# Kernel tuning notes

Measured on AMD Instinct MI355X. Metric: run time of the kernel, lower is better.

The kernel has to match this reference:

```python
import jax, jax.numpy as jnp
import numpy as np
from jax import lax

S, B, T, H, FH, FU = 8, 256, 90, 256, 14, 76
IN_H, IN_F, IN_U = 16, 16, 4


def _cell(x, h, c, Wih, Whh, b):
    # x:[S,B,in] h,c:[S,B,H] Wih:[S,4H,in] Whh:[S,4H,H] b:[S,4H]
    g = jnp.einsum('sbi,sgi->sbg', x, Wih) + jnp.einsum('sbh,sgh->sbg', h, Whh) + b[:, None, :]
    i, f, gg, o = jnp.split(g, 4, axis=-1)
    c = jax.nn.sigmoid(f) * c + jax.nn.sigmoid(i) * jnp.tanh(gg)
    h = jax.nn.sigmoid(o) * jnp.tanh(c)
    return h, c


def _encode(x_seq, params):
    # x_seq:[T,S,B,in]; stacked LSTM, zero initial state (torch nn.LSTM default)
    hs, cs = [], []
    inp = x_seq
    for (Wih, Whh, b) in params:
        h0 = jnp.zeros((x_seq.shape[1], x_seq.shape[2], Whh.shape[-1]), x_seq.dtype)

        def step(carry, x, Wih=Wih, Whh=Whh, b=b):
            h, c = _cell(x, carry[0], carry[1], Wih, Whh, b)
            return (h, c), h

        (h, c), inp = lax.scan(step, (h0, h0), inp)
        hs.append(h); cs.append(c)
    return jnp.stack(hs), jnp.stack(cs)  # [L,S,B,H]


def _decode(x_seq, params, h0, c0, level, win, wout, gW, gb, adj, flow_std):
    L = len(params)

    def step(carry, x):
        hs, cs, lev = carry
        inp = x
        nh, nc = [], []
        for l in range(L):
            h, c = _cell(inp, hs[l], cs[l], *params[l])
            inp = h; nh.append(h); nc.append(c)
        # headers_in: Linear(H+1 -> H, no bias) + ReLU (dropout is eval no-op)
        feat = jnp.concatenate([inp, lev], axis=-1)            # [S,B,H+1]
        hin = jax.nn.relu(jnp.einsum('sbf,shf->sbh', feat, win))
        # GraphConvolution: adj @ (X W) + b over the site axis
        graphed = jnp.einsum('st,tbk->sbk', adj, jnp.einsum('sbh,hk->sbk', hin, gW)) + gb
        # headers_out: ReLU + Linear(H -> 1, no bias)
        flow = jnp.einsum('sbh,soh->sbo', jax.nn.relu(graphed), wout)  # [S,B,1]
        lev = lev + flow * flow_std[:, None, None]
        return (jnp.stack(nh), jnp.stack(nc), lev), flow[..., 0]
    (hs, cs, lev), flows = lax.scan(step, (h0, c0, level), x_seq)
    return hs, cs, lev, flows  # flows: [T,S,B]


def setup_inputs() -> dict:
    key = jax.random.key(0)
    ks = iter(jax.random.split(key, 40))
    sc = 1.0 / np.sqrt(H)

    def u(shape):
        return jax.random.uniform(next(ks), shape, jnp.float32, -sc, sc)

    inp = {
        'x_d': jax.random.normal(next(ks), (S, B, T, IN_H), jnp.float32),
        'x_f': jax.random.normal(next(ks), (S, B, FH, IN_F), jnp.float32),
        'x_ff': jax.random.normal(next(ks), (S, B, FU, IN_U), jnp.float32),
        'level0': jax.random.uniform(next(ks), (S, B, 1), jnp.float32),
        'flow_std': jax.random.uniform(next(ks), (S,), jnp.float32, 0.5, 2.0),
    }
    # adjacency: chain edges + self loops (diag=True, digraph=False)
    adj = np.zeros((S, S), dtype=np.float32)
    for i in range(S - 1):
        adj[i, i + 1] = 1.0
    adj += np.eye(S, dtype=np.float32)
    inp['adj'] = jnp.asarray(adj)
    for pfx, in0 in [('enc', IN_H), ('df', IN_F), ('du', IN_U)]:
        inp[pfx + '_Wih0'] = u((S, 4 * H, in0))
        inp[pfx + '_Whh0'] = u((S, 4 * H, H))
        inp[pfx + '_b0'] = u((S, 4 * H))
        inp[pfx + '_Wih1'] = u((S, 4 * H, H))
        inp[pfx + '_Whh1'] = u((S, 4 * H, H))
        inp[pfx + '_b1'] = u((S, 4 * H))
    inp['win'] = u((S, H, H + 1))
    inp['wout'] = u((S, 1, H))
    inp['gW'] = u((H, H))
    inp['gb'] = u((H,))
    return inp


def reference(x_d, x_f, x_ff, level0, flow_std, adj,
              enc_Wih0, enc_Whh0, enc_b0, enc_Wih1, enc_Whh1, enc_b1,
              df_Wih0, df_Whh0, df_b0, df_Wih1, df_Whh1, df_b1,
              du_Wih0, du_Whh0, du_b0, du_Wih1, du_Whh1, du_b1,
              win, wout, gW, gb):
    enc_p = [(enc_Wih0, enc_Whh0, enc_b0), (enc_Wih1, enc_Whh1, enc_b1)]
    df_p = [(df_Wih0, df_Whh0, df_b0), (df_Wih1, df_Whh1, df_b1)]
    du_p = [(du_Wih0, du_Whh0, du_b0), (du_Wih1, du_Whh1, du_b1)]
    # encode historic sequence per site
    h, c = _encode(jnp.transpose(x_d, (2, 0, 1, 3)), enc_p)
    # forecast-horizon decode with graph mixing each step
    h, c, lev, f1 = _decode(jnp.transpose(x_f, (2, 0, 1, 3)), df_p, h, c,
                            level0, win, wout, gW, gb, adj, flow_std)
    # future-horizon decode continues from the same state
    h, c, lev, f2 = _decode(jnp.transpose(x_ff, (2, 0, 1, 3)), du_p, h, c,
                            lev, win, wout, gW, gb, adj, flow_std)
    flows = jnp.concatenate([f1, f2], axis=0)      # [FH+FU, S, B]
    return jnp.transpose(flows, (2, 0, 1))         # [B, target_horizon, S]
```

## Files before the change

### kernel.cpp

```cpp
#include <hip/hip_runtime.h>

typedef unsigned short u16;
typedef __bf16 bf16_t;
typedef bf16_t bf16x8 __attribute__((ext_vector_type(8)));
typedef float f32x4 __attribute__((ext_vector_type(4)));
typedef unsigned int u32x4 __attribute__((ext_vector_type(4)));

#define DEV static __device__ __forceinline__
#define RLX __ATOMIC_RELAXED
#define AGT __HIP_MEMORY_SCOPE_AGENT

DEV u16 f2bf(float f){ unsigned u = __float_as_uint(f); return (u16)((u + 0x7fffu + ((u>>16)&1u))>>16); }
DEV float bf2f(u16 b){ return __uint_as_float(((unsigned)b)<<16); }
DEV float sigf(float x){ return 1.0f/(1.0f+__expf(-x)); }
DEV float tanhf_(float x){ float e = __expf(2.0f*x); return 1.0f - 2.0f/(e+1.0f); }

union FragU { bf16x8 v; u16 u[8]; u32x4 q; };

DEV void ldg16_nw(u32x4 r[16], const void* b0, const void* b1){
  asm volatile(
    "global_load_dwordx4 %0,  %16, off sc0 sc1\n\t"
    "global_load_dwordx4 %1,  %16, off offset:64 sc0 sc1\n\t"
    "global_load_dwordx4 %2,  %16, off offset:128 sc0 sc1\n\t"
    "global_load_dwordx4 %3,  %16, off offset:192 sc0 sc1\n\t"
    "global_load_dwordx4 %4,  %16, off offset:256 sc0 sc1\n\t"
    "global_load_dwordx4 %5,  %16, off offset:320 sc0 sc1\n\t"
    "global_load_dwordx4 %6,  %16, off offset:384 sc0 sc1\n\t"
    "global_load_dwordx4 %7,  %16, off offset:448 sc0 sc1\n\t"
    "global_load_dwordx4 %8,  %17, off sc0 sc1\n\t"
    "global_load_dwordx4 %9,  %17, off offset:64 sc0 sc1\n\t"
    "global_load_dwordx4 %10, %17, off offset:128 sc0 sc1\n\t"
    "global_load_dwordx4 %11, %17, off offset:192 sc0 sc1\n\t"
    "global_load_dwordx4 %12, %17, off offset:256 sc0 sc1\n\t"
    "global_load_dwordx4 %13, %17, off offset:320 sc0 sc1\n\t"
    "global_load_dwordx4 %14, %17, off offset:384 sc0 sc1\n\t"
    "global_load_dwordx4 %15, %17, off offset:448 sc0 sc1"
    : "=&v"(r[0]), "=&v"(r[1]), "=&v"(r[2]), "=&v"(r[3]),
      "=&v"(r[4]), "=&v"(r[5]), "=&v"(r[6]), "=&v"(r[7]),
      "=&v"(r[8]), "=&v"(r[9]), "=&v"(r[10]), "=&v"(r[11]),
      "=&v"(r[12]), "=&v"(r[13]), "=&v"(r[14]), "=&v"(r[15])
    : "v"(b0), "v"(b1)
    : "memory");
}
DEV void wait_vm16(){ asm volatile("s_waitcnt vmcnt(16)" ::: "memory"); __builtin_amdgcn_sched_barrier(0); }
DEV void wait_vm0(){ asm volatile("s_waitcnt vmcnt(0)" ::: "memory"); __builtin_amdgcn_sched_barrier(0); }

DEV void ldg8f_sc(u32x4 r[8], float& lv, const void* b0, const float* lp){
  asm volatile(
    "global_load_dwordx4 %0, %9, off sc0 sc1\n\t"
    "global_load_dwordx4 %1, %9, off offset:64 sc0 sc1\n\t"
    "global_load_dwordx4 %2, %9, off offset:128 sc0 sc1\n\t"
    "global_load_dwordx4 %3, %9, off offset:192 sc0 sc1\n\t"
    "global_load_dwordx4 %4, %9, off offset:256 sc0 sc1\n\t"
    "global_load_dwordx4 %5, %9, off offset:320 sc0 sc1\n\t"
    "global_load_dwordx4 %6, %9, off offset:384 sc0 sc1\n\t"
    "global_load_dwordx4 %7, %9, off offset:448 sc0 sc1\n\t"
    "global_load_dword %8, %10, off sc0 sc1\n\t"
    "s_waitcnt vmcnt(0)"
    : "=&v"(r[0]), "=&v"(r[1]), "=&v"(r[2]), "=&v"(r[3]),
      "=&v"(r[4]), "=&v"(r[5]), "=&v"(r[6]), "=&v"(r[7]), "=&v"(lv)
    : "v"(b0), "v"(lp) : "memory");
}
DEV float ldf_sc(const float* p){
  float r;
  asm volatile("global_load_dword %0, %1, off sc0 sc1\n\ts_waitcnt vmcnt(0)"
               : "=&v"(r) : "v"(p) : "memory");
  return r;
}
DEV void stg16_sc(void* p, u32x4 v){
  asm volatile("global_store_dwordx4 %0, %1, off sc0 sc1" :: "v"(p), "v"(v) : "memory");
}
DEV void stf_sc(float* p, float v){
  asm volatile("global_store_dword %0, %1, off sc0 sc1" :: "v"(p), "v"(v) : "memory");
}
DEV unsigned ld_spin_ic(const unsigned* p){
  unsigned r;
  asm volatile("global_load_dword %0, %1, off sc0 sc1\n\ts_waitcnt vmcnt(0)"
               : "=&v"(r) : "v"(p) : "memory");
  return r;
}

struct PArgs {
  const u16 *whh0[3], *wih0p[3], *whh1[3], *wih1[3];
  const float *b0[3], *b1[3];
  const float *x[3];
  const u16 *winH; const float *winLev;
  const u16 *gT;
  const float *gb, *wout, *adj, *fstd;
  u16 *h0a, *h0b, *h1a, *h1b;
  u16 *hgA, *hgB;
  float *levA, *levB;
  float *out;
  unsigned *bar;
  int T[3]; int IN[3];
};

DEV void pinW256(const u16* Wsite, int gt, u16* lds, int tid){
#pragma unroll
  for (int it = 0; it < 8; ++it){
    int flat = it*512 + tid;
    int n = flat >> 5, ks = flat & 31;
    int j = (n >> 5)*256 + gt*32 + (n & 31);
    bf16x8 v = *reinterpret_cast<const bf16x8*>(Wsite + (size_t)j*256 + ks*8);
    int sl = ks ^ (n & 7);
    *reinterpret_cast<bf16x8*>(lds + n*256 + sl*8) = v;
  }
}
DEV void pinWp(const u16* wpSite, int gt, u16* lds, int tid){
  int n = tid >> 2, ks = tid & 3;
  int j = (n >> 5)*256 + gt*32 + (n & 31);
  bf16x8 v = *reinterpret_cast<const bf16x8*>(wpSite + (size_t)j*32 + ks*8);
  int sl = ks ^ (n & 3);
  *reinterpret_cast<bf16x8*>(lds + n*32 + sl*8) = v;
}
DEV void pinWin(const u16* winH, int s, int gt, u16* lds, int tid){
#pragma unroll
  for (int it = 0; it < 2; ++it){
    int flat = it*512 + tid;
    int nn = flat >> 5, ks = flat & 31;
    bf16x8 v = *reinterpret_cast<const bf16x8*>(winH + ((size_t)s*256 + gt*32 + nn)*256 + ks*8);
    int sl = ks ^ (nn & 7);
    *reinterpret_cast<bf16x8*>(lds + nn*256 + sl*8) = v;
  }
}

DEV void seg_mfma(const u16* ldsW, const u32x4 a[16], f32x4 acc[2][4],
                  int l15, int l4, int nh){
#pragma unroll
  for (int ck = 0; ck < 8; ++ck){
#pragma unroll
    for (int mf = 0; mf < 2; ++mf){
      FragU af; af.q = a[mf*8 + ck];
#pragma unroll
      for (int q = 0; q < 4; ++q){
        int n = q*32 + nh*16 + l15;
        int sl = (ck*4 + l4) ^ (n & 7);
        acc[mf][q] = __builtin_amdgcn_mfma_f32_16x16x32_bf16(
            af.v, *reinterpret_cast<const bf16x8*>(ldsW + n*256 + sl*8), acc[mf][q], 0,0,0);
      }
    }
  }
}

DEV void cell_epi2(const float bb[4], float* cR, u16* hOutSite,
                   int rowBase, int hcb, int lane, u16* wscr, const f32x4 acc[2][4]){
  int l15 = lane & 15, l4 = lane >> 4;
#pragma unroll
  for (int mf = 0; mf < 2; ++mf)
#pragma unroll
    for (int r = 0; r < 4; ++r){
      float gi = acc[mf][0][r] + bb[0];
      float gf = acc[mf][1][r] + bb[1];
      float gg = acc[mf][2][r] + bb[2];
      float go = acc[mf][3][r] + bb[3];
      float cn = sigf(gf)*cR[mf*4+r] + sigf(gi)*tanhf_(gg);
      cR[mf*4+r] = cn;
      wscr[(mf*16 + l4*4 + r)*16 + l15] = f2bf(sigf(go)*tanhf_(cn));
    }
  asm volatile("s_waitcnt lgkmcnt(0)" ::: "memory");
  u32x4 v = *reinterpret_cast<const u32x4*>(wscr + lane*8);
  stg16_sc(hOutSite + (size_t)(rowBase + (lane>>1))*256 + hcb + (lane&1)*8, v);
}

__global__ __launch_bounds__(512, 2) void k_persist(PArgs A){
  extern __shared__ char smem[];
  u16* lds0 = (u16*)smem;
  u16* lds1 = (u16*)(smem + 65536);
  u16* ldsWin = (u16*)(smem + 65536 + 8192);
  u16* scratch = (u16*)(smem + 131072);
  float (*red)[16] = (float(*)[16])(smem + 139264);
  __shared__ unsigned pollE[8], pollD[8];

  const int bid = blockIdx.x, tid = threadIdx.x;
  const int w = tid >> 6, lane = tid & 63, l15 = lane & 15, l4 = lane >> 4;
  const int s = bid & 7, fam = (bid >> 3) & 1, sub = bid >> 4;
  const int bt = sub & 1, gt = sub >> 1;
  const int mt = w & 3, nh = w >> 2;
  const int rowBase = bt*128 + mt*32;
  const int hcb = gt*32 + nh*16;
  const size_t sOff = (size_t)s*65536;
  u16* wscr = scratch + w*512;

  auto offA = [](int ss, int bb){ return (unsigned)((ss*2 + bb)*64); };
  auto offB = [](int ss, int bb){ return (unsigned)(1024 + (ss*2 + bb)*64); };
  if (tid == 0){
    pollE[0] = offA(s, bt); pollE[1] = offB(s, bt);
#pragma unroll
    for (int i = 2; i < 8; ++i) pollE[i] = pollE[0];
    if (fam == 0){
      pollD[0] = offA(s, bt);
      pollD[1] = offB(s, 0); pollD[2] = offB(s, 1);
      pollD[3] = (s > 0) ? offB(s-1, 0) : pollD[0];
      pollD[4] = (s > 0) ? offB(s-1, 1) : pollD[0];
      pollD[5] = pollD[0]; pollD[6] = pollD[0]; pollD[7] = pollD[0];
    } else {
      pollD[0] = offA(s, 0); pollD[1] = offA(s, 1);
      pollD[2] = offB(s, 0); pollD[3] = offB(s, 1);
      if (s < 7){
        pollD[4] = offA(s+1, 0); pollD[5] = offA(s+1, 1);
        pollD[6] = offB(s+1, 0); pollD[7] = offB(s+1, 1);
      } else {
        pollD[4] = pollD[0]; pollD[5] = pollD[0];
        pollD[6] = pollD[0]; pollD[7] = pollD[0];
      }
    }
  }
  unsigned* myCnt = A.bar + ((fam == 0) ? offA(s, bt) : offB(s, bt));
  __syncthreads();

  float cR[8];
#pragma unroll
  for (int i = 0; i < 8; ++i) cR[i] = 0.f;

  unsigned gen = 0;
  const int gb0[3] = {0, 90, 104};

  for (int ph = 0; ph < 3; ++ph){
    const int T = A.T[ph];
    const int IN = A.IN[ph];
    const bool dec = (ph > 0);
    const int SS = T + (dec ? 3 : 1);
    const int tdb = (ph == 2) ? 14 : 0;

    float bb[4];
    if (fam == 0){
      pinW256(A.whh0[ph] + (size_t)s*262144, gt, lds0, tid);
      pinWp  (A.wih0p[ph] + (size_t)s*32768, gt, lds1, tid);
      pinWin (A.winH, s, gt, ldsWin, tid);
      const float* bS = A.b0[ph] + s*1024;
#pragma unroll
      for (int g = 0; g < 4; ++g) bb[g] = bS[g*256 + hcb + l15];
    } else {
      pinW256(A.whh1[ph] + (size_t)s*262144, gt, lds0, tid);
      pinW256(A.wih1[ph] + (size_t)s*262144, gt, lds1, tid);
      const float* bS = A.b1[ph] + s*1024;
#pragma unroll
      for (int g = 0; g < 4; ++g) bb[g] = bS[g*256 + hcb + l15];
    }
    __syncthreads();

    for (int ss = 0; ss < SS; ++ss){
      if (w == 0){
        unsigned off = (dec ? pollD : pollE)[lane & 7];
        const unsigned* p = A.bar + off;
        unsigned tgt = 8u * gen;
        for (;;){
          unsigned v = ld_spin_ic(p);
          if (__all((int)(v >= tgt))) break;
          __builtin_amdgcn_s_sleep(1);
        }
      }
      __syncthreads();

      if (fam == 0){
        if (ss < T){
          int t = ss, g0 = gb0[ph] + t;
          const u16* h0in = ((g0 & 1) ? A.h0b : A.h0a) + sOff;
          u16* h0out = ((g0 & 1) ? A.h0a : A.h0b) + sOff;
          f32x4 acc[2][4];
#pragma unroll
          for (int mf = 0; mf < 2; ++mf)
#pragma unroll
            for (int q = 0; q < 4; ++q) acc[mf][q] = (f32x4){0.f,0.f,0.f,0.f};
          u32x4 a[16];
          ldg16_nw(a, h0in + (size_t)(rowBase + l15)*256 + l4*8,
                      h0in + (size_t)(rowBase + 16 + l15)*256 + l4*8);
          FragU xa[2];
#pragma unroll
          for (int mf = 0; mf < 2; ++mf){
#pragma unroll
            for (int e = 0; e < 8; ++e) xa[mf].u[e] = 0;
            const float* xrow = A.x[ph] + ((size_t)(s*256 + rowBase + mf*16 + l15)*T + t)*IN;
            if (IN == 16){
              if (l4 < 2){
                float4 u0 = reinterpret_cast<const float4*>(xrow)[l4*2];
                float4 u1 = reinterpret_cast<const float4*>(xrow)[l4*2+1];
                xa[mf].u[0]=f2bf(u0.x); xa[mf].u[1]=f2bf(u0.y); xa[mf].u[2]=f2bf(u0.z); xa[mf].u[3]=f2bf(u0.w);
                xa[mf].u[4]=f2bf(u1.x); xa[mf].u[5]=f2bf(u1.y); xa[mf].u[6]=f2bf(u1.z); xa[mf].u[7]=f2bf(u1.w);
              }
            } else {
              if (l4 == 0){
                float4 u0 = *reinterpret_cast<const float4*>(xrow);
                xa[mf].u[0]=f2bf(u0.x); xa[mf].u[1]=f2bf(u0.y); xa[mf].u[2]=f2bf(u0.z); xa[mf].u[3]=f2bf(u0.w);
              }
            }
          }
          wait_vm0();
          seg_mfma(lds0, a, acc, l15, l4, nh);
#pragma unroll
          for (int mf = 0; mf < 2; ++mf)
#pragma unroll
            for (int q = 0; q < 4; ++q){
              int n = q*32 + nh*16 + l15;
              int sl = l4 ^ (n & 3);
              acc[mf][q] = __builtin_amdgcn_mfma_f32_16x16x32_bf16(
                  xa[mf].v, *reinterpret_cast<const bf16x8*>(lds1 + n*32 + sl*8), acc[mf][q], 0,0,0);
            }
          cell_epi2(bb, cR, h0out, rowBase, hcb, lane, wscr, acc);
        }
        if (dec){
          int th = ss - 2;
          if (th >= 0 && th < T){
            int g = gb0[ph] + th, tdec = tdb + th;
            const u16* h1cur = ((g & 1) ? A.h1a : A.h1b) + sOff;
            u16* hg = ((tdec & 1) ? A.hgB : A.hgA) + sOff;
            f32x4 a2[2];
            a2[0] = (f32x4){0.f,0.f,0.f,0.f}; a2[1] = a2[0];
            u32x4 a[16];
            ldg16_nw(a, h1cur + (size_t)(rowBase + l15)*256 + l4*8,
                        h1cur + (size_t)(rowBase + 16 + l15)*256 + l4*8);
            wait_vm0();
#pragma unroll
            for (int ck = 0; ck < 8; ++ck)
#pragma unroll
              for (int mf = 0; mf < 2; ++mf){
                FragU af; af.q = a[mf*8 + ck];
                int n = nh*16 + l15;
                int sl = (ck*4 + l4) ^ (n & 7);
                a2[mf] = __builtin_amdgcn_mfma_f32_16x16x32_bf16(
                    af.v, *reinterpret_cast<const bf16x8*>(ldsWin + n*256 + sl*8), a2[mf], 0,0,0);
              }
#pragma unroll
            for (int mf = 0; mf < 2; ++mf)
#pragma unroll
              for (int r = 0; r < 4; ++r)
                wscr[(mf*16 + l4*4 + r)*16 + l15] = f2bf(a2[mf][r]);
            asm volatile("s_waitcnt lgkmcnt(0)" ::: "memory");
            u32x4 v = *reinterpret_cast<const u32x4*>(wscr + lane*8);
            stg16_sc(hg + (size_t)(rowBase + (lane>>1))*256 + hcb + (lane&1)*8, v);
          }
        }
      } else {
        int t = ss - 1;
        if (t >= 0 && t < T){
          int g = gb0[ph] + t;
          const u16* h1in = ((g & 1) ? A.h1b : A.h1a) + sOff;
          u16* h1out = ((g & 1) ? A.h1a : A.h1b) + sOff;
          const u16* h0cur = ((g & 1) ? A.h0a : A.h0b) + sOff;
          f32x4 acc[2][4];
#pragma unroll
          for (int mf = 0; mf < 2; ++mf)
#pragma unroll
            for (int q = 0; q < 4; ++q) acc[mf][q] = (f32x4){0.f,0.f,0.f,0.f};
          u32x4 a0[16], a1[16];
          ldg16_nw(a0, h1in + (size_t)(rowBase + l15)*256 + l4*8,
                       h1in + (size_t)(rowBase + 16 + l15)*256 + l4*8);
          ldg16_nw(a1, h0cur + (size_t)(rowBase + l15)*256 + l4*8,
                       h0cur + (size_t)(rowBase + 16 + l15)*256 + l4*8);
          wait_vm16();
          seg_mfma(lds0, a0, acc, l15, l4, nh);
          wait_vm0();
          seg_mfma(lds1, a1, acc, l15, l4, nh);
          cell_epi2(bb, cR, h1out, rowBase, hcb, lane, wscr, acc);
        }
        if (dec){
          int tgl = ss - 3;
          if (tgl >= 0 && tgl < T){
            int tg = tdb + tgl;
            const u16* hgb16 = (tg & 1) ? A.hgB : A.hgA;
            const float* levc = (tg & 1) ? A.levB : A.levA;
            float* levn = (tg & 1) ? A.levA : A.levB;
            int brow0 = sub*16;
            f32x4 acc[2];
            acc[0] = (f32x4){0.f,0.f,0.f,0.f}; acc[1] = acc[0];
            for (int ts = 0; ts < 8; ++ts){
              float av = A.adj[s*8 + ts];
              if (av == 0.f) continue;
              float lv;
              u32x4 hv[8];
              ldg8f_sc(hv, lv, hgb16 + (size_t)ts*65536 + (size_t)(brow0 + l15)*256 + l4*8,
                       levc + ts*256 + brow0 + l15);
              const float* wlB = A.winLev + ts*256 + l4*8;
#pragma unroll
              for (int ck = 0; ck < 8; ++ck){
                FragU hr; hr.q = hv[ck];
                float4 w0 = *reinterpret_cast<const float4*>(wlB + ck*32);
                float4 w1 = *reinterpret_cast<const float4*>(wlB + ck*32 + 4);
                float wls[8] = {w0.x,w0.y,w0.z,w0.w,w1.x,w1.y,w1.z,w1.w};
                FragU af;
#pragma unroll
                for (int e = 0; e < 8; ++e)
                  af.u[e] = f2bf(fmaxf(bf2f(hr.u[e]) + lv*wls[e], 0.f) * av);
#pragma unroll
                for (int q = 0; q < 2; ++q){
                  int n = (w*2+q)*16 + l15;
                  bf16x8 bfr = *reinterpret_cast<const bf16x8*>(A.gT + (size_t)n*256 + ck*32 + l4*8);
                  acc[q] = __builtin_amdgcn_mfma_f32_16x16x32_bf16(af.v, bfr, acc[q], 0,0,0);
                }
              }
            }
            float part[4] = {0.f,0.f,0.f,0.f};
            const float* woS = A.wout + s*256;
#pragma unroll
            for (int q = 0; q < 2; ++q){
              int m = (w*2+q)*16 + l15;
              float gbv = A.gb[m], wo = woS[m];
#pragma unroll
              for (int r = 0; r < 4; ++r) part[r] += fmaxf(acc[q][r] + gbv, 0.f) * wo;
            }
#pragma unroll
            for (int d = 1; d < 16; d <<= 1)
#pragma unroll
              for (int r = 0; r < 4; ++r) part[r] += __shfl_xor(part[r], d, 64);
            if (l15 == 0)
#pragma unroll
              for (int r = 0; r < 4; ++r) red[w][l4*4+r] = part[r];
            __syncthreads();
            if (tid < 16){
              float flow = 0.f;
#pragma unroll
              for (int ww = 0; ww < 8; ++ww) flow += red[ww][tid];
              int b = brow0 + tid;
              A.out[(size_t)b*720 + tg*8 + s] = flow;
              float lvo = ldf_sc(levc + s*256 + b);
              stf_sc(levn + s*256 + b, lvo + flow * A.fstd[s]);
            }
          }
        }
      }
      asm volatile("s_waitcnt vmcnt(0)" ::: "memory");
      __syncthreads();
      if (tid == 0) __hip_atomic_fetch_add(myCnt, 1u, RLX, AGT);
      ++gen;
    }
  }
}

struct Cvt9Args { const float* s[9]; u16* d[9]; };
__global__ void k_cvt9(Cvt9Args A){
  size_t i = (size_t)blockIdx.x*256 + threadIdx.x;
  int t = (int)(i >> 21); size_t r = i & 2097151u;
  A.d[t][r] = f2bf(A.s[t][r]);
}
struct Pad3Args { const float* s[3]; u16* d[3]; int kx[3]; };
__global__ void k_pad3(Pad3Args A){
  size_t i = (size_t)blockIdx.x*256 + threadIdx.x;
  int t = (int)(i >> 18); int r = (int)(i & 262143u);
  int row = r >> 5, col = r & 31;
  int kx = A.kx[t];
  A.d[t][r] = (col < kx) ? f2bf(A.s[t][(size_t)row*kx + col]) : (u16)0;
}
__global__ void k_win(const float* win, u16* winH, float* winLev){
  size_t i = (size_t)blockIdx.x*256 + threadIdx.x;
  if (i >= (size_t)8*256*257) return;
  int k = (int)(i % 257); size_t sm = i / 257;
  float v = win[i];
  if (k < 256) winH[sm*256 + k] = f2bf(v);
  else winLev[sm] = v;
}
__global__ void k_gt(const float* gW, u16* gT){
  int i = blockIdx.x*256 + threadIdx.x;
  int h = i >> 8, k = i & 255;
  gT[(size_t)k*256 + h] = f2bf(gW[i]);
}

extern "C" void kernel_launch(void* const* d_in, const int* in_sizes, int n_in,
                              void* d_out, int out_size, void* d_ws, size_t ws_size,
                              hipStream_t stream){
  const float* x_d    = (const float*)d_in[0];
  const float* x_f    = (const float*)d_in[1];
  const float* x_ff   = (const float*)d_in[2];
  const float* level0 = (const float*)d_in[3];
  const float* fstd   = (const float*)d_in[4];
  const float* adj    = (const float*)d_in[5];
  const float* W[18];
  for (int i = 0; i < 18; i++) W[i] = (const float*)d_in[6+i];
  const float* win  = (const float*)d_in[24];
  const float* wout = (const float*)d_in[25];
  const float* gW   = (const float*)d_in[26];
  const float* gb   = (const float*)d_in[27];

  char* base = (char*)d_ws;
  size_t off = 0;
  auto alloc = [&](size_t bytes)->void*{
    void* r = base + off;
    off += (bytes + 255) & ~(size_t)255;
    return r;
  };
  u16* wb[9]; for (int i = 0; i < 9; i++) wb[i] = (u16*)alloc((size_t)2097152*2);
  u16* wp[3]; for (int i = 0; i < 3; i++) wp[i] = (u16*)alloc((size_t)262144*2);
  u16* winH = (u16*)alloc((size_t)524288*2);
  u16* gT   = (u16*)alloc((size_t)65536*2);
  float* winLev = (float*)alloc((size_t)2048*4);
  u16* h0a = (u16*)alloc((size_t)524288*2);
  u16* h0b = (u16*)alloc((size_t)524288*2);
  u16* h1a = (u16*)alloc((size_t)524288*2);
  u16* h1b = (u16*)alloc((size_t)524288*2);
  u16* hgA = (u16*)alloc((size_t)524288*2);
  u16* hgB = (u16*)alloc((size_t)524288*2);
  float* levA = (float*)alloc((size_t)2048*4);
  float* levB = (float*)alloc((size_t)2048*4);
  unsigned* bar = (unsigned*)alloc(16384);

  Cvt9Args c9;
  const float* c9s[9] = { W[1], W[4], W[3],  W[7], W[10], W[9],  W[13], W[16], W[15] };
  for (int i = 0; i < 9; i++){ c9.s[i] = c9s[i]; c9.d[i] = wb[i]; }
  k_cvt9<<<73728,256,0,stream>>>(c9);

  Pad3Args p3;
  const float* p3s[3] = { W[0], W[6], W[12] };
  int kx3[3] = {16,16,4};
  for (int i = 0; i < 3; i++){ p3.s[i] = p3s[i]; p3.d[i] = wp[i]; p3.kx[i] = kx3[i]; }
  k_pad3<<<3072,256,0,stream>>>(p3);

  k_win<<<2057,256,0,stream>>>(win, winH, winLev);
  k_gt<<<256,256,0,stream>>>(gW, gT);

  (void)hipMemsetAsync(h0a, 0, (size_t)524288*2, stream);
  (void)hipMemsetAsync(h1a, 0, (size_t)524288*2, stream);
  (void)hipMemsetAsync(bar, 0, 16384, stream);
  (void)hipMemcpyAsync(levA, level0, (size_t)2048*4, hipMemcpyDeviceToDevice, stream);

  PArgs A;
  for (int ph = 0; ph < 3; ++ph){
    A.whh0[ph] = wb[ph*3+0];
    A.whh1[ph] = wb[ph*3+1];
    A.wih1[ph] = wb[ph*3+2];
    A.wih0p[ph] = wp[ph];
  }
  A.b0[0] = W[2];  A.b1[0] = W[5];
  A.b0[1] = W[8];  A.b1[1] = W[11];
  A.b0[2] = W[14]; A.b1[2] = W[17];
  A.x[0] = x_d; A.x[1] = x_f; A.x[2] = x_ff;
  A.winH = winH; A.winLev = winLev;
  A.gT = gT; A.gb = gb; A.wout = wout; A.adj = adj; A.fstd = fstd;
  A.h0a = h0a; A.h0b = h0b; A.h1a = h1a; A.h1b = h1b;
  A.hgA = hgA; A.hgB = hgB;
  A.levA = levA; A.levB = levB;
  A.out = (float*)d_out;
  A.bar = bar;
  A.T[0] = 90; A.T[1] = 14; A.T[2] = 76;
  A.IN[0] = 16; A.IN[1] = 16; A.IN[2] = 4;

  const int smemBytes = 139776;
  (void)hipFuncSetAttribute((const void*)k_persist, hipFuncAttributeMaxDynamicSharedMemorySize, smemBytes);
  k_persist<<<dim3(256), dim3(512), smemBytes, stream>>>(A);
}
```

Before: 3.235 ms.

## Use L2-coherent loads/stores for per-site hidden state when all site blocks share an XCD

At kernel start each block records its XCC ID in a per-site bitmask and waits on a grid-wide counter. Once all blocks have arrived, a site whose blocks all sit on one XCD switches its hidden-state loads and stores from system-coherent (sc0 sc1) to L2-scope (sc0) cache policy. This avoids bypassing the shared L2 for recurrent state exchanged only among blocks on the same XCD. It adds a one-time grid barrier and template duplication of the main loop. Correctness relies on the runtime XCD placement check, and the graph-mixing buffer keeps the coherent path.

After: 4.317 ms. +33.4%, slower.

```diff
diff --git a/kernel.cpp b/kernel.cpp
--- a/kernel.cpp
+++ b/kernel.cpp
@@ -17,31 +17,34 @@
 
 union FragU { bf16x8 v; u16 u[8]; u32x4 q; };
 
-DEV void ldg16_nw(u32x4 r[16], const void* b0, const void* b1){
-  asm volatile(
-    "global_load_dwordx4 %0,  %16, off sc0 sc1\n\t"
-    "global_load_dwordx4 %1,  %16, off offset:64 sc0 sc1\n\t"
-    "global_load_dwordx4 %2,  %16, off offset:128 sc0 sc1\n\t"
-    "global_load_dwordx4 %3,  %16, off offset:192 sc0 sc1\n\t"
-    "global_load_dwordx4 %4,  %16, off offset:256 sc0 sc1\n\t"
-    "global_load_dwordx4 %5,  %16, off offset:320 sc0 sc1\n\t"
-    "global_load_dwordx4 %6,  %16, off offset:384 sc0 sc1\n\t"
-    "global_load_dwordx4 %7,  %16, off offset:448 sc0 sc1\n\t"
-    "global_load_dwordx4 %8,  %17, off sc0 sc1\n\t"
-    "global_load_dwordx4 %9,  %17, off offset:64 sc0 sc1\n\t"
-    "global_load_dwordx4 %10, %17, off offset:128 sc0 sc1\n\t"
-    "global_load_dwordx4 %11, %17, off offset:192 sc0 sc1\n\t"
-    "global_load_dwordx4 %12, %17, off offset:256 sc0 sc1\n\t"
-    "global_load_dwordx4 %13, %17, off offset:320 sc0 sc1\n\t"
-    "global_load_dwordx4 %14, %17, off offset:384 sc0 sc1\n\t"
-    "global_load_dwordx4 %15, %17, off offset:448 sc0 sc1"
-    : "=&v"(r[0]), "=&v"(r[1]), "=&v"(r[2]), "=&v"(r[3]),
-      "=&v"(r[4]), "=&v"(r[5]), "=&v"(r[6]), "=&v"(r[7]),
-      "=&v"(r[8]), "=&v"(r[9]), "=&v"(r[10]), "=&v"(r[11]),
-      "=&v"(r[12]), "=&v"(r[13]), "=&v"(r[14]), "=&v"(r[15])
-    : "v"(b0), "v"(b1)
-    : "memory");
-}
+#define DEF_LDG16(NAME, SC)                                            \
+DEV void NAME(u32x4 r[16], const void* b0, const void* b1){            \
+  asm volatile(                                                        \
+    "global_load_dwordx4 %0,  %16, off " SC "\n\t"                     \
+    "global_load_dwordx4 %1,  %16, off offset:64 " SC "\n\t"           \
+    "global_load_dwordx4 %2,  %16, off offset:128 " SC "\n\t"          \
+    "global_load_dwordx4 %3,  %16, off offset:192 " SC "\n\t"          \
+    "global_load_dwordx4 %4,  %16, off offset:256 " SC "\n\t"          \
+    "global_load_dwordx4 %5,  %16, off offset:320 " SC "\n\t"          \
+    "global_load_dwordx4 %6,  %16, off offset:384 " SC "\n\t"          \
+    "global_load_dwordx4 %7,  %16, off offset:448 " SC "\n\t"          \
+    "global_load_dwordx4 %8,  %17, off " SC "\n\t"                     \
+    "global_load_dwordx4 %9,  %17, off offset:64 " SC "\n\t"           \
+    "global_load_dwordx4 %10, %17, off offset:128 " SC "\n\t"          \
+    "global_load_dwordx4 %11, %17, off offset:192 " SC "\n\t"          \
+    "global_load_dwordx4 %12, %17, off offset:256 " SC "\n\t"          \
+    "global_load_dwordx4 %13, %17, off offset:320 " SC "\n\t"          \
+    "global_load_dwordx4 %14, %17, off offset:384 " SC "\n\t"          \
+    "global_load_dwordx4 %15, %17, off offset:448 " SC                 \
+    : "=&v"(r[0]), "=&v"(r[1]), "=&v"(r[2]), "=&v"(r[3]),              \
+      "=&v"(r[4]), "=&v"(r[5]), "=&v"(r[6]), "=&v"(r[7]),              \
+      "=&v"(r[8]), "=&v"(r[9]), "=&v"(r[10]), "=&v"(r[11]),            \
+      "=&v"(r[12]), "=&v"(r[13]), "=&v"(r[14]), "=&v"(r[15])           \
+    : "v"(b0), "v"(b1) : "memory");                                    \
+}
+DEF_LDG16(ldg16_ic, "sc0 sc1")
+DEF_LDG16(ldg16_l2, "sc0")
+
 DEV void wait_vm16(){ asm volatile("s_waitcnt vmcnt(16)" ::: "memory"); __builtin_amdgcn_sched_barrier(0); }
 DEV void wait_vm0(){ asm volatile("s_waitcnt vmcnt(0)" ::: "memory"); __builtin_amdgcn_sched_barrier(0); }
 
@@ -67,8 +70,11 @@
                : "=&v"(r) : "v"(p) : "memory");
   return r;
 }
-DEV void stg16_sc(void* p, u32x4 v){
+DEV void stg16_ic(void* p, u32x4 v){
   asm volatile("global_store_dwordx4 %0, %1, off sc0 sc1" :: "v"(p), "v"(v) : "memory");
+}
+DEV void stg16_l2(void* p, u32x4 v){
+  asm volatile("global_store_dwordx4 %0, %1, off sc0" :: "v"(p), "v"(v) : "memory");
 }
 DEV void stf_sc(float* p, float v){
   asm volatile("global_store_dword %0, %1, off sc0 sc1" :: "v"(p), "v"(v) : "memory");
@@ -78,6 +84,13 @@
   asm volatile("global_load_dword %0, %1, off sc0 sc1\n\ts_waitcnt vmcnt(0)"
                : "=&v"(r) : "v"(p) : "memory");
   return r;
+}
+
+template<bool L2H> DEV void ldg16h(u32x4 r[16], const void* b0, const void* b1){
+  if constexpr (L2H) ldg16_l2(r, b0, b1); else ldg16_ic(r, b0, b1);
+}
+template<bool L2H> DEV void stg16h(void* p, u32x4 v){
+  if constexpr (L2H) stg16_l2(p, v); else stg16_ic(p, v);
 }
 
 struct PArgs {
@@ -142,6 +155,7 @@
   }
 }
 
+template<bool L2H>
 DEV void cell_epi2(const float bb[4], float* cR, u16* hOutSite,
                    int rowBase, int hcb, int lane, u16* wscr, const f32x4 acc[2][4]){
   int l15 = lane & 15, l4 = lane >> 4;
@@ -159,11 +173,11 @@
     }
   asm volatile("s_waitcnt lgkmcnt(0)" ::: "memory");
   u32x4 v = *reinterpret_cast<const u32x4*>(wscr + lane*8);
-  stg16_sc(hOutSite + (size_t)(rowBase + (lane>>1))*256 + hcb + (lane&1)*8, v);
-}
-
-__global__ __launch_bounds__(512, 2) void k_persist(PArgs A){
-  extern __shared__ char smem[];
+  stg16h<L2H>(hOutSite + (size_t)(rowBase + (lane>>1))*256 + hcb + (lane&1)*8, v);
+}
+
+template<bool L2H>
+DEV void mainLoop(const PArgs& A, char* smem, int bid, int tid){
   u16* lds0 = (u16*)smem;
   u16* lds1 = (u16*)(smem + 65536);
   u16* ldsWin = (u16*)(smem + 65536 + 8192);
@@ -171,7 +185,6 @@
   float (*red)[16] = (float(*)[16])(smem + 139264);
   __shared__ unsigned pollE[8], pollD[8];
 
-  const int bid = blockIdx.x, tid = threadIdx.x;
   const int w = tid >> 6, lane = tid & 63, l15 = lane & 15, l4 = lane >> 4;
   const int s = bid & 7, fam = (bid >> 3) & 1, sub = bid >> 4;
   const int bt = sub & 1, gt = sub >> 1;
@@ -263,8 +276,8 @@
 #pragma unroll
             for (int q = 0; q < 4; ++q) acc[mf][q] = (f32x4){0.f,0.f,0.f,0.f};
           u32x4 a[16];
-          ldg16_nw(a, h0in + (size_t)(rowBase + l15)*256 + l4*8,
-                      h0in + (size_t)(rowBase + 16 + l15)*256 + l4*8);
+          ldg16h<L2H>(a, h0in + (size_t)(rowBase + l15)*256 + l4*8,
+                         h0in + (size_t)(rowBase + 16 + l15)*256 + l4*8);
           FragU xa[2];
 #pragma unroll
           for (int mf = 0; mf < 2; ++mf){
@@ -296,7 +309,7 @@
               acc[mf][q] = __builtin_amdgcn_mfma_f32_16x16x32_bf16(
                   xa[mf].v, *reinterpret_cast<const bf16x8*>(lds1 + n*32 + sl*8), acc[mf][q], 0,0,0);
             }
-          cell_epi2(bb, cR, h0out, rowBase, hcb, lane, wscr, acc);
+          cell_epi2<L2H>(bb, cR, h0out, rowBase, hcb, lane, wscr, acc);
         }
         if (dec){
           int th = ss - 2;
@@ -307,8 +320,8 @@
             f32x4 a2[2];
             a2[0] = (f32x4){0.f,0.f,0.f,0.f}; a2[1] = a2[0];
             u32x4 a[16];
-            ldg16_nw(a, h1cur + (size_t)(rowBase + l15)*256 + l4*8,
-                        h1cur + (size_t)(rowBase + 16 + l15)*256 + l4*8);
+            ldg16h<L2H>(a, h1cur + (size_t)(rowBase + l15)*256 + l4*8,
+                           h1cur + (size_t)(rowBase + 16 + l15)*256 + l4*8);
             wait_vm0();
 #pragma unroll
             for (int ck = 0; ck < 8; ++ck)
@@ -327,7 +340,7 @@
                 wscr[(mf*16 + l4*4 + r)*16 + l15] = f2bf(a2[mf][r]);
             asm volatile("s_waitcnt lgkmcnt(0)" ::: "memory");
             u32x4 v = *reinterpret_cast<const u32x4*>(wscr + lane*8);
-            stg16_sc(hg + (size_t)(rowBase + (lane>>1))*256 + hcb + (lane&1)*8, v);
+            stg16_ic(hg + (size_t)(rowBase + (lane>>1))*256 + hcb + (lane&1)*8, v);
           }
         }
       } else {
@@ -343,15 +356,15 @@
 #pragma unroll
             for (int q = 0; q < 4; ++q) acc[mf][q] = (f32x4){0.f,0.f,0.f,0.f};
           u32x4 a0[16], a1[16];
-          ldg16_nw(a0, h1in + (size_t)(rowBase + l15)*256 + l4*8,
-                       h1in + (size_t)(rowBase + 16 + l15)*256 + l4*8);
-          ldg16_nw(a1, h0cur + (size_t)(rowBase + l15)*256 + l4*8,
-                       h0cur + (size_t)(rowBase + 16 + l15)*256 + l4*8);
+          ldg16h<L2H>(a0, h1in + (size_t)(rowBase + l15)*256 + l4*8,
+                          h1in + (size_t)(rowBase + 16 + l15)*256 + l4*8);
+          ldg16h<L2H>(a1, h0cur + (size_t)(rowBase + l15)*256 + l4*8,
+                          h0cur + (size_t)(rowBase + 16 + l15)*256 + l4*8);
           wait_vm16();
           seg_mfma(lds0, a0, acc, l15, l4, nh);
           wait_vm0();
           seg_mfma(lds1, a1, acc, l15, l4, nh);
-          cell_epi2(bb, cR, h1out, rowBase, hcb, lane, wscr, acc);
+          cell_epi2<L2H>(bb, cR, h1out, rowBase, hcb, lane, wscr, acc);
         }
         if (dec){
           int tgl = ss - 3;
@@ -424,6 +437,25 @@
       ++gen;
     }
   }
+}
+
+__global__ __launch_bounds__(512, 2) void k_persist(PArgs A){
+  extern __shared__ char smem[];
+  __shared__ unsigned shFlag;
+  const int bid = blockIdx.x, tid = threadIdx.x;
+  const int s = bid & 7;
+  unsigned xcd = 0;
+  asm volatile("s_getreg_b32 %0, hwreg(HW_REG_XCC_ID)" : "=s"(xcd));
+  if (tid == 0){
+    __hip_atomic_fetch_or(A.bar + 2112 + s*64, 1u << (xcd & 31), RLX, AGT);
+    __hip_atomic_fetch_add(A.bar + 2048, 1u, RLX, AGT);
+    while (__hip_atomic_load(A.bar + 2048, RLX, AGT) < 256u) __builtin_amdgcn_s_sleep(2);
+    unsigned m = __hip_atomic_load(A.bar + 2112 + s*64, RLX, AGT);
+    shFlag = (__popc(m) == 1) ? 1u : 0u;
+  }
+  __syncthreads();
+  if (shFlag) mainLoop<true>(A, smem, bid, tid);
+  else        mainLoop<false>(A, smem, bid, tid);
 }
 
 struct Cvt9Args { const float* s[9]; u16* d[9]; };
```

## Retile per-wave MFMA work to 16 rows by all 32 gate columns

Applied to the files above, without the earlier changes.

Each wave previously owned 32 batch rows and 16 hidden columns. It now owns 16 batch rows and all 32 hidden columns of the block's gate tile. Each wave therefore loads half as many h activation rows from global memory per step, but reads twice as many weight fragments from LDS. The intent is to cut global and L2 load latency on the recurrent critical path. The trade-off is more LDS weight traffic per wave, and the epilogue store layout changes to match.

Measured after the change: 2.864 ms. -11.5%, faster.

```diff
diff --git a/kernel.cpp b/kernel.cpp
--- a/kernel.cpp
+++ b/kernel.cpp
@@ -17,32 +17,21 @@
 
 union FragU { bf16x8 v; u16 u[8]; u32x4 q; };
 
-DEV void ldg16_nw(u32x4 r[16], const void* b0, const void* b1){
+DEV void ldg8_nw(u32x4 r[8], const void* b0){
   asm volatile(
-    "global_load_dwordx4 %0,  %16, off sc0 sc1\n\t"
-    "global_load_dwordx4 %1,  %16, off offset:64 sc0 sc1\n\t"
-    "global_load_dwordx4 %2,  %16, off offset:128 sc0 sc1\n\t"
-    "global_load_dwordx4 %3,  %16, off offset:192 sc0 sc1\n\t"
-    "global_load_dwordx4 %4,  %16, off offset:256 sc0 sc1\n\t"
-    "global_load_dwordx4 %5,  %16, off offset:320 sc0 sc1\n\t"
-    "global_load_dwordx4 %6,  %16, off offset:384 sc0 sc1\n\t"
-    "global_load_dwordx4 %7,  %16, off offset:448 sc0 sc1\n\t"
-    "global_load_dwordx4 %8,  %17, off sc0 sc1\n\t"
-    "global_load_dwordx4 %9,  %17, off offset:64 sc0 sc1\n\t"
-    "global_load_dwordx4 %10, %17, off offset:128 sc0 sc1\n\t"
-    "global_load_dwordx4 %11, %17, off offset:192 sc0 sc1\n\t"
-    "global_load_dwordx4 %12, %17, off offset:256 sc0 sc1\n\t"
-    "global_load_dwordx4 %13, %17, off offset:320 sc0 sc1\n\t"
-    "global_load_dwordx4 %14, %17, off offset:384 sc0 sc1\n\t"
-    "global_load_dwordx4 %15, %17, off offset:448 sc0 sc1"
+    "global_load_dwordx4 %0, %8, off sc0 sc1\n\t"
+    "global_load_dwordx4 %1, %8, off offset:64 sc0 sc1\n\t"
+    "global_load_dwordx4 %2, %8, off offset:128 sc0 sc1\n\t"
+    "global_load_dwordx4 %3, %8, off offset:192 sc0 sc1\n\t"
+    "global_load_dwordx4 %4, %8, off offset:256 sc0 sc1\n\t"
+    "global_load_dwordx4 %5, %8, off offset:320 sc0 sc1\n\t"
+    "global_load_dwordx4 %6, %8, off offset:384 sc0 sc1\n\t"
+    "global_load_dwordx4 %7, %8, off offset:448 sc0 sc1"
     : "=&v"(r[0]), "=&v"(r[1]), "=&v"(r[2]), "=&v"(r[3]),
-      "=&v"(r[4]), "=&v"(r[5]), "=&v"(r[6]), "=&v"(r[7]),
-      "=&v"(r[8]), "=&v"(r[9]), "=&v"(r[10]), "=&v"(r[11]),
-      "=&v"(r[12]), "=&v"(r[13]), "=&v"(r[14]), "=&v"(r[15])
-    : "v"(b0), "v"(b1)
-    : "memory");
-}
-DEV void wait_vm16(){ asm volatile("s_waitcnt vmcnt(16)" ::: "memory"); __builtin_amdgcn_sched_barrier(0); }
+      "=&v"(r[4]), "=&v"(r[5]), "=&v"(r[6]), "=&v"(r[7])
+    : "v"(b0) : "memory");
+}
+DEV void wait_vm8(){ asm volatile("s_waitcnt vmcnt(8)" ::: "memory"); __builtin_amdgcn_sched_barrier(0); }
 DEV void wait_vm0(){ asm volatile("s_waitcnt vmcnt(0)" ::: "memory"); __builtin_amdgcn_sched_barrier(0); }
 
 DEV void ldg8f_sc(u32x4 r[8], float& lv, const void* b0, const float* lp){
@@ -124,42 +113,38 @@
   }
 }
 
-DEV void seg_mfma(const u16* ldsW, const u32x4 a[16], f32x4 acc[2][4],
-                  int l15, int l4, int nh){
+DEV void seg_mfma8(const u16* ldsW, const u32x4 a[8], f32x4 acc[8], int l15, int l4){
 #pragma unroll
   for (int ck = 0; ck < 8; ++ck){
-#pragma unroll
-    for (int mf = 0; mf < 2; ++mf){
-      FragU af; af.q = a[mf*8 + ck];
-#pragma unroll
-      for (int q = 0; q < 4; ++q){
-        int n = q*32 + nh*16 + l15;
-        int sl = (ck*4 + l4) ^ (n & 7);
-        acc[mf][q] = __builtin_amdgcn_mfma_f32_16x16x32_bf16(
-            af.v, *reinterpret_cast<const bf16x8*>(ldsW + n*256 + sl*8), acc[mf][q], 0,0,0);
-      }
+    FragU af; af.q = a[ck];
+#pragma unroll
+    for (int q = 0; q < 8; ++q){
+      int n = (q >> 1)*32 + (q & 1)*16 + l15;
+      int sl = (ck*4 + l4) ^ (n & 7);
+      acc[q] = __builtin_amdgcn_mfma_f32_16x16x32_bf16(
+          af.v, *reinterpret_cast<const bf16x8*>(ldsW + n*256 + sl*8), acc[q], 0,0,0);
     }
   }
 }
 
-DEV void cell_epi2(const float bb[4], float* cR, u16* hOutSite,
-                   int rowBase, int hcb, int lane, u16* wscr, const f32x4 acc[2][4]){
+DEV void cell_epi(const float bb[4][2], float* cR, u16* hOutSite,
+                  int rowBase, int hc0, int lane, u16* wscr, const f32x4 acc[8]){
   int l15 = lane & 15, l4 = lane >> 4;
 #pragma unroll
-  for (int mf = 0; mf < 2; ++mf)
+  for (int h2 = 0; h2 < 2; ++h2)
 #pragma unroll
     for (int r = 0; r < 4; ++r){
-      float gi = acc[mf][0][r] + bb[0];
-      float gf = acc[mf][1][r] + bb[1];
-      float gg = acc[mf][2][r] + bb[2];
-      float go = acc[mf][3][r] + bb[3];
-      float cn = sigf(gf)*cR[mf*4+r] + sigf(gi)*tanhf_(gg);
-      cR[mf*4+r] = cn;
-      wscr[(mf*16 + l4*4 + r)*16 + l15] = f2bf(sigf(go)*tanhf_(cn));
+      float gi = acc[0 + h2][r] + bb[0][h2];
+      float gf = acc[2 + h2][r] + bb[1][h2];
+      float gg = acc[4 + h2][r] + bb[2][h2];
+      float go = acc[6 + h2][r] + bb[3][h2];
+      float cn = sigf(gf)*cR[h2*4+r] + sigf(gi)*tanhf_(gg);
+      cR[h2*4+r] = cn;
+      wscr[(l4*4 + r)*32 + h2*16 + l15] = f2bf(sigf(go)*tanhf_(cn));
     }
   asm volatile("s_waitcnt lgkmcnt(0)" ::: "memory");
-  u32x4 v = *reinterpret_cast<const u32x4*>(wscr + lane*8);
-  stg16_sc(hOutSite + (size_t)(rowBase + (lane>>1))*256 + hcb + (lane&1)*8, v);
+  u32x4 v = *reinterpret_cast<const u32x4*>(wscr + (lane>>2)*32 + (lane&3)*8);
+  stg16_sc(hOutSite + (size_t)(rowBase + (lane>>2))*256 + hc0 + (lane&3)*8, v);
 }
 
 __global__ __launch_bounds__(512, 2) void k_persist(PArgs A){
@@ -175,14 +160,13 @@
   const int w = tid >> 6, lane = tid & 63, l15 = lane & 15, l4 = lane >> 4;
   const int s = bid & 7, fam = (bid >> 3) & 1, sub = bid >> 4;
   const int bt = sub & 1, gt = sub >> 1;
-  const int mt = w & 3, nh = w >> 2;
-  const int rowBase = bt*128 + mt*32;
-  const int hcb = gt*32 + nh*16;
+  const int rowBase = bt*128 + w*16;
+  const int hc0 = gt*32;
   const size_t sOff = (size_t)s*65536;
   u16* wscr = scratch + w*512;
 
-  auto offA = [](int ss, int bb){ return (unsigned)((ss*2 + bb)*64); };
-  auto offB = [](int ss, int bb){ return (unsigned)(1024 + (ss*2 + bb)*64); };
+  auto offA = [](int ss, int bb_){ return (unsigned)((ss*2 + bb_)*64); };
+  auto offB = [](int ss, int bb_){ return (unsigned)(1024 + (ss*2 + bb_)*64); };
   if (tid == 0){
     pollE[0] = offA(s, bt); pollE[1] = offB(s, bt);
 #pragma unroll
@@ -222,20 +206,20 @@
     const int SS = T + (dec ? 3 : 1);
     const int tdb = (ph == 2) ? 14 : 0;
 
-    float bb[4];
+    float bb[4][2];
     if (fam == 0){
       pinW256(A.whh0[ph] + (size_t)s*262144, gt, lds0, tid);
       pinWp  (A.wih0p[ph] + (size_t)s*32768, gt, lds1, tid);
       pinWin (A.winH, s, gt, ldsWin, tid);
       const float* bS = A.b0[ph] + s*1024;
 #pragma unroll
-      for (int g = 0; g < 4; ++g) bb[g] = bS[g*256 + hcb + l15];
+      for (int g = 0; g < 4; ++g){ bb[g][0] = bS[g*256 + hc0 + l15]; bb[g][1] = bS[g*256 + hc0 + 16 + l15]; }
     } else {
       pinW256(A.whh1[ph] + (size_t)s*262144, gt, lds0, tid);
       pinW256(A.wih1[ph] + (size_t)s*262144, gt, lds1, tid);
       const float* bS = A.b1[ph] + s*1024;
 #pragma unroll
-      for (int g = 0; g < 4; ++g) bb[g] = bS[g*256 + hcb + l15];
+      for (int g = 0; g < 4; ++g){ bb[g][0] = bS[g*256 + hc0 + l15]; bb[g][1] = bS[g*256 + hc0 + 16 + l15]; }
     }
     __syncthreads();
 
@@ -257,46 +241,40 @@
           int t = ss, g0 = gb0[ph] + t;
           const u16* h0in = ((g0 & 1) ? A.h0b : A.h0a) + sOff;
           u16* h0out = ((g0 & 1) ? A.h0a : A.h0b) + sOff;
-          f32x4 acc[2][4];
-#pragma unroll
-          for (int mf = 0; mf < 2; ++mf)
-#pragma unroll
-            for (int q = 0; q < 4; ++q) acc[mf][q] = (f32x4){0.f,0.f,0.f,0.f};
-          u32x4 a[16];
-          ldg16_nw(a, h0in + (size_t)(rowBase + l15)*256 + l4*8,
-                      h0in + (size_t)(rowBase + 16 + l15)*256 + l4*8);
-          FragU xa[2];
-#pragma unroll
-          for (int mf = 0; mf < 2; ++mf){
-#pragma unroll
-            for (int e = 0; e < 8; ++e) xa[mf].u[e] = 0;
-            const float* xrow = A.x[ph] + ((size_t)(s*256 + rowBase + mf*16 + l15)*T + t)*IN;
+          f32x4 acc[8];
+#pragma unroll
+          for (int q = 0; q < 8; ++q) acc[q] = (f32x4){0.f,0.f,0.f,0.f};
+          u32x4 a[8];
+          ldg8_nw(a, h0in + (size_t)(rowBase + l15)*256 + l4*8);
+          FragU xa;
+#pragma unroll
+          for (int e = 0; e < 8; ++e) xa.u[e] = 0;
+          {
+            const float* xrow = A.x[ph] + ((size_t)(s*256 + rowBase + l15)*T + t)*IN;
             if (IN == 16){
               if (l4 < 2){
                 float4 u0 = reinterpret_cast<const float4*>(xrow)[l4*2];
                 float4 u1 = reinterpret_cast<const float4*>(xrow)[l4*2+1];
-                xa[mf].u[0]=f2bf(u0.x); xa[mf].u[1]=f2bf(u0.y); xa[mf].u[2]=f2bf(u0.z); xa[mf].u[3]=f2bf(u0.w);
-                xa[mf].u[4]=f2bf(u1.x); xa[mf].u[5]=f2bf(u1.y); xa[mf].u[6]=f2bf(u1.z); xa[mf].u[7]=f2bf(u1.w);
+                xa.u[0]=f2bf(u0.x); xa.u[1]=f2bf(u0.y); xa.u[2]=f2bf(u0.z); xa.u[3]=f2bf(u0.w);
+                xa.u[4]=f2bf(u1.x); xa.u[5]=f2bf(u1.y); xa.u[6]=f2bf(u1.z); xa.u[7]=f2bf(u1.w);
               }
             } else {
               if (l4 == 0){
                 float4 u0 = *reinterpret_cast<const float4*>(xrow);
-                xa[mf].u[0]=f2bf(u0.x); xa[mf].u[1]=f2bf(u0.y); xa[mf].u[2]=f2bf(u0.z); xa[mf].u[3]=f2bf(u0.w);
+                xa.u[0]=f2bf(u0.x); xa.u[1]=f2bf(u0.y); xa.u[2]=f2bf(u0.z); xa.u[3]=f2bf(u0.w);
               }
             }
           }
           wait_vm0();
-          seg_mfma(lds0, a, acc, l15, l4, nh);
-#pragma unroll
-          for (int mf = 0; mf < 2; ++mf)
-#pragma unroll
-            for (int q = 0; q < 4; ++q){
-              int n = q*32 + nh*16 + l15;
-              int sl = l4 ^ (n & 3);
-              acc[mf][q] = __builtin_amdgcn_mfma_f32_16x16x32_bf16(
-                  xa[mf].v, *reinterpret_cast<const bf16x8*>(lds1 + n*32 + sl*8), acc[mf][q], 0,0,0);
-            }
-          cell_epi2(bb, cR, h0out, rowBase, hcb, lane, wscr, acc);
+          seg_mfma8(lds0, a, acc, l15, l4);
+#pragma unroll
+          for (int q = 0; q < 8; ++q){
+            int n = (q >> 1)*32 + (q & 1)*16 + l15;
+            int sl = l4 ^ (n & 3);
+            acc[q] = __builtin_amdgcn_mfma_f32_16x16x32_bf16(
+                xa.v, *reinterpret_cast<const bf16x8*>(lds1 + n*32 + sl*8), acc[q], 0,0,0);
+          }
+          cell_epi(bb, cR, h0out, rowBase, hc0, lane, wscr, acc);
         }
         if (dec){
           int th = ss - 2;
@@ -306,28 +284,28 @@
             u16* hg = ((tdec & 1) ? A.hgB : A.hgA) + sOff;
             f32x4 a2[2];
             a2[0] = (f32x4){0.f,0.f,0.f,0.f}; a2[1] = a2[0];
-            u32x4 a[16];
-            ldg16_nw(a, h1cur + (size_t)(rowBase + l15)*256 + l4*8,
-                        h1cur + (size_t)(rowBase + 16 + l15)*256 + l4*8);
+            u32x4 a[8];
+            ldg8_nw(a, h1cur + (size_t)(rowBase + l15)*256 + l4*8);
             wait_vm0();
 #pragma unroll
-            for (int ck = 0; ck < 8; ++ck)
-#pragma unroll
-              for (int mf = 0; mf < 2; ++mf){
-                FragU af; af.q = a[mf*8 + ck];
-                int n = nh*16 + l15;
+            for (int ck = 0; ck < 8; ++ck){
+              FragU af; af.q = a[ck];
+#pragma unroll
+              for (int q = 0; q < 2; ++q){
+                int n = q*16 + l15;
                 int sl = (ck*4 + l4) ^ (n & 7);
-                a2[mf] = __builtin_amdgcn_mfma_f32_16x16x32_bf16(
-                    af.v, *reinterpret_cast<const bf16x8*>(ldsWin + n*256 + sl*8), a2[mf], 0,0,0);
+                a2[q] = __builtin_amdgcn_mfma_f32_16x16x32_bf16(
+                    af.v, *reinterpret_cast<const bf16x8*>(ldsWin + n*256 + sl*8), a2[q], 0,0,0);
               }
-#pragma unroll
-            for (int mf = 0; mf < 2; ++mf)
+            }
+#pragma unroll
+            for (int q = 0; q < 2; ++q)
 #pragma unroll
               for (int r = 0; r < 4; ++r)
-                wscr[(mf*16 + l4*4 + r)*16 + l15] = f2bf(a2[mf][r]);
+                wscr[(l4*4 + r)*32 + q*16 + l15] = f2bf(a2[q][r]);
             asm volatile("s_waitcnt lgkmcnt(0)" ::: "memory");
-            u32x4 v = *reinterpret_cast<const u32x4*>(wscr + lane*8);
-            stg16_sc(hg + (size_t)(rowBase + (lane>>1))*256 + hcb + (lane&1)*8, v);
+            u32x4 v = *reinterpret_cast<const u32x4*>(wscr + (lane>>2)*32 + (lane&3)*8);
+            stg16_sc(hg + (size_t)(rowBase + (lane>>2))*256 + hc0 + (lane&3)*8, v);
           }
         }
       } else {
@@ -337,21 +315,17 @@
           const u16* h1in = ((g & 1) ? A.h1b : A.h1a) + sOff;
           u16* h1out = ((g & 1) ? A.h1a : A.h1b) + sOff;
           const u16* h0cur = ((g & 1) ? A.h0a : A.h0b) + sOff;
-          f32x4 acc[2][4];
-#pragma unroll
-          for (int mf = 0; mf < 2; ++mf)
-#pragma unroll
-            for (int q = 0; q < 4; ++q) acc[mf][q] = (f32x4){0.f,0.f,0.f,0.f};
-          u32x4 a0[16], a1[16];
-          ldg16_nw(a0, h1in + (size_t)(rowBase + l15)*256 + l4*8,
-                       h1in + (size_t)(rowBase + 16 + l15)*256 + l4*8);
-          ldg16_nw(a1, h0cur + (size_t)(rowBase + l15)*256 + l4*8,
-                       h0cur + (size_t)(rowBase + 16 + l15)*256 + l4*8);
-          wait_vm16();
-          seg_mfma(lds0, a0, acc, l15, l4, nh);
+          f32x4 acc[8];
+#pragma unroll
+          for (int q = 0; q < 8; ++q) acc[q] = (f32x4){0.f,0.f,0.f,0.f};
+          u32x4 a0[8], a1[8];
+          ldg8_nw(a0, h1in + (size_t)(rowBase + l15)*256 + l4*8);
+          ldg8_nw(a1, h0cur + (size_t)(rowBase + l15)*256 + l4*8);
+          wait_vm8();
+          seg_mfma8(lds0, a0, acc, l15, l4);
           wait_vm0();
-          seg_mfma(lds1, a1, acc, l15, l4, nh);
-          cell_epi2(bb, cR, h1out, rowBase, hcb, lane, wscr, acc);
+          seg_mfma8(lds1, a1, acc, l15, l4);
+          cell_epi(bb, cR, h1out, rowBase, hc0, lane, wscr, acc);
         }
         if (dec){
           int tgl = ss - 3;
```
